# Performance work log

Measured on AMD Instinct MI355X. Metric: run time of the kernel, lower is better.

Reference implementation:

```python
import jax, jax.numpy as jnp
import numpy as np

EMBED_DIM = 768
FFN_DIM = 3072
N_WIRES = 10


def setup_inputs() -> dict:
    key = jax.random.key(0)
    ks = jax.random.split(key, 7)
    x = jax.random.normal(ks[0], (8, 2048, EMBED_DIM), dtype=jnp.float32)
    # map_to_wires: nn.Linear(embed_dim, n_wires, bias=False) -> weight [n_wires, embed_dim]
    W_map = jax.random.normal(ks[1], (N_WIRES, EMBED_DIM), dtype=jnp.float32) / np.sqrt(EMBED_DIM)
    # trainable RY rotation angles, one per wire
    theta = jax.random.uniform(ks[2], (N_WIRES,), dtype=jnp.float32, minval=-np.pi, maxval=np.pi)
    W1 = jax.random.normal(ks[3], (FFN_DIM, N_WIRES), dtype=jnp.float32) / np.sqrt(N_WIRES)
    b1 = jnp.zeros((FFN_DIM,), dtype=jnp.float32)
    W2 = jax.random.normal(ks[4], (EMBED_DIM, FFN_DIM), dtype=jnp.float32) / np.sqrt(FFN_DIM)
    b2 = jnp.zeros((EMBED_DIM,), dtype=jnp.float32)
    return {"x": x, "W_map": W_map, "theta": theta, "W1": W1, "b1": b1, "W2": W2, "b2": b2}


def reference(x, W_map, theta, W1, b1, W2, b2):
    batch, seq_len, embed_dim = x.shape
    x_flat = x.reshape(batch * seq_len, embed_dim)            # [F, E]
    x_wires = x_flat @ W_map.T                                 # [F, W]
    # Quantum circuit: per wire i, state RY(theta_i) RX(x_i) |0>.
    # All gates are single-qubit on the |0...0> product state, so the
    # register stays a product state and <Z_i> reduces exactly to
    # cos(theta_i) * cos(x_i) (same math as the full 2^n statevector sim).
    q_out = jnp.cos(theta)[None, :] * jnp.cos(x_wires)         # [F, W]
    h = jax.nn.relu(q_out @ W1.T + b1)                         # [F, FFN]
    out = h @ W2.T + b2                                        # [F, E]
    return out.reshape(batch, seq_len, embed_dim)
```

## Files before the change

### kernel.cpp

```cpp
#include <hip/hip_runtime.h>
#include <hip/hip_bf16.h>


typedef __attribute__((ext_vector_type(4))) float f32x4;
typedef __attribute__((ext_vector_type(8))) short bf16x8;

#define F_TOTAL 16384
#define E_DIM   768
#define FFN     3072

static __device__ __forceinline__ unsigned short f2bf(float f) {
    union { float f; unsigned int i; } v; v.f = f;
    unsigned int r = v.i + 0x7FFFu + ((v.i >> 16) & 1u);
    return (unsigned short)(r >> 16);
}
static __device__ __forceinline__ unsigned int pkbf(float a, float b) {
    __hip_bfloat162 h2 = __float22bfloat162_rn(float2{a, b});
    union { __hip_bfloat162 h; unsigned int u; } v; v.h = h2; return v.u;
}
static __device__ __forceinline__ void gload16(const void* g, void* l) {
    __builtin_amdgcn_global_load_lds((const __attribute__((address_space(1))) unsigned int*)g,
                                     (__attribute__((address_space(3))) unsigned int*)l,
                                     16, 0, 0);
}

__global__ __launch_bounds__(256) void kPre(const float* __restrict__ x,
                                            const float* __restrict__ wm,
                                            const float* __restrict__ th,
                                            const float* __restrict__ w1,
                                            const float* __restrict__ b1,
                                            const float* __restrict__ w2,
                                            unsigned short* __restrict__ w2b,
                                            unsigned short* __restrict__ w1p,
                                            unsigned short* __restrict__ qp) {
    __shared__ float wms[10 * 768];
    const int bid = (int)blockIdx.x;
    const int tid = (int)threadIdx.x;

    if (bid < 768) {
        const int n = bid;
#pragma unroll
        for (int c0 = 0; c0 < 2; ++c0) {
            int c = tid + c0 * 256;
            if (c < 384) {
                const float4* src = (const float4*)(w2 + (size_t)n * FFN + c * 8);
                float4 a = src[0], b = src[1];
                bf16x8 v;
                v[0] = (short)f2bf(a.x); v[1] = (short)f2bf(a.y);
                v[2] = (short)f2bf(a.z); v[3] = (short)f2bf(a.w);
                v[4] = (short)f2bf(b.x); v[5] = (short)f2bf(b.y);
                v[6] = (short)f2bf(b.z); v[7] = (short)f2bf(b.w);
                *(bf16x8*)(w2b + (size_t)n * FFN + (size_t)(c ^ (n & 7)) * 8) = v;
            }
        }
        return;
    }
    if (bid < 780) {
        int k = (bid - 768) * 256 + tid;
        if (k < FFN) {
            float r[32];
#pragma unroll
            for (int w = 0; w < 10; ++w) r[w] = w1[k * 10 + w];
            r[10] = b1[k];
#pragma unroll
            for (int w = 11; w < 32; ++w) r[w] = 0.f;
#pragma unroll
            for (int c = 0; c < 4; ++c) {
                bf16x8 v;
#pragma unroll
                for (int e = 0; e < 8; ++e) v[e] = (short)f2bf(r[c * 8 + e]);
                *(bf16x8*)(w1p + (size_t)k * 32 + (size_t)((c ^ (k & 3)) * 8)) = v;
            }
        }
        return;
    }

    for (int i = tid; i < 10 * 768; i += 256) wms[i] = wm[i];
    __syncthreads();

    const int wv = tid >> 6, l = tid & 63;
    const int mbase = (bid - 780) * 16 + wv * 4;
    const float thv = (l < 10) ? th[l] : 0.f;
    const float cth = __cosf(thv);

#pragma unroll
    for (int r = 0; r < 4; ++r) {
        const int m = mbase + r;
        const float4* xp = (const float4*)(x + (size_t)m * E_DIM);
        const float4 xa = xp[l], xb = xp[64 + l], xc = xp[128 + l];
        float s[10];
#pragma unroll
        for (int w = 0; w < 10; ++w) {
            const float4* wp = (const float4*)(wms + w * E_DIM);
            const float4 wa = wp[l], wb = wp[64 + l], wc = wp[128 + l];
            float t0 = xa.x * wa.x;
            float t1 = xa.y * wa.y;
            t0 = fmaf(xa.z, wa.z, t0); t1 = fmaf(xa.w, wa.w, t1);
            t0 = fmaf(xb.x, wb.x, t0); t1 = fmaf(xb.y, wb.y, t1);
            t0 = fmaf(xb.z, wb.z, t0); t1 = fmaf(xb.w, wb.w, t1);
            t0 = fmaf(xc.x, wc.x, t0); t1 = fmaf(xc.y, wc.y, t1);
            t0 = fmaf(xc.z, wc.z, t0); t1 = fmaf(xc.w, wc.w, t1);
            s[w] = t0 + t1;
        }
#pragma unroll
        for (int w = 0; w < 10; ++w) {
            float v = s[w];
            v += __shfl_xor(v, 1);  v += __shfl_xor(v, 2);  v += __shfl_xor(v, 4);
            v += __shfl_xor(v, 8);  v += __shfl_xor(v, 16); v += __shfl_xor(v, 32);
            s[w] = v;
        }
        if (l < 32) {
            float sv = 0.f;
#pragma unroll
            for (int w = 0; w < 10; ++w) sv = (l == w) ? s[w] : sv;
            float val = (l < 10) ? (cth * __cosf(sv)) : ((l == 10) ? 1.0f : 0.f);
            qp[(size_t)m * 32 + (size_t)((((l >> 3) ^ (m & 3)) * 8) + (l & 7))] = f2bf(val);
        }
    }
}

__global__ __launch_bounds__(512, 4) void kG(const unsigned short* __restrict__ w2b,
                                             const float* __restrict__ b2,
                                             const unsigned short* __restrict__ qp,
                                             const unsigned short* __restrict__ w1p,
                                             float* __restrict__ outp) {
    __shared__ __align__(16) unsigned short w2s[2][192 * 64];
    __shared__ __align__(16) unsigned short hs[128 * 64];

    const int tid = (int)threadIdx.x;
    const int wv = tid >> 6, l = tid & 63;
    const int bid = (int)blockIdx.x;
    const int x8 = bid & 7, yb = bid >> 3;
    const int m0 = ((x8 & 1) * 64 + yb) * 128;
    const int n0 = (x8 >> 1) * 192;

    const int rw = tid >> 3, cw = tid & 7;
    const int wr = wv >> 2, wc = wv & 3;
    const int par = wv & 1;

    int hwo[4];
    {
        const int hm = wv * 16 + (l & 15);
        const int kb = (l >> 4) * 4;
#pragma unroll
        for (int ki = 0; ki < 4; ++ki) {
            int k = ki * 16 + kb;
            int c = k >> 3;
            hwo[ki] = hm * 64 + ((c ^ (hm & 7)) * 8) + (k & 7);
        }
    }

#define STAGE(BUF, KT) do { int k0_ = (KT) * 64;                                   \
    _Pragma("unroll") for (int i_ = 0; i_ < 3; ++i_) {                             \
        int r_ = i_ * 64 + rw;                                                     \
        gload16(w2b + (size_t)(n0 + r_) * FFN + k0_ + (size_t)cw * 8,              \
                (unsigned short*)w2s[BUF] + i_ * 4096 + wv * 512); } } while (0)

#define LOADW1(D, KT, KI) do {                                                     \
    const unsigned short* a_ = w1p + (size_t)((KT) * 64 + (KI) * 16 + (l & 15)) * 32 \
                                   + (size_t)(((l >> 4) ^ (l & 3)) * 8);           \
    asm volatile("global_load_dwordx4 %0, %1, off" : "=v"(D) : "v"(a_)); } while (0)

    bf16x8 aq;
    {
        const unsigned short* qa = qp + (size_t)(m0 + wv * 16 + (l & 15)) * 32
                                      + (size_t)(((l >> 4) ^ (l & 3)) * 8);
        asm volatile("global_load_dwordx4 %0, %1, off" : "=v"(aq) : "v"(qa));
    }
    bf16x8 f0, f1, f2, f3, g0, g1, g2, g3;
    STAGE(0, 0);
    LOADW1(f0, 0, 0); LOADW1(f1, 0, 1); LOADW1(f2, 0, 2); LOADW1(f3, 0, 3);

    const f32x4 z4 = {0.f, 0.f, 0.f, 0.f};
    f32x4 acc[4][3];
#pragma unroll
    for (int a = 0; a < 4; ++a)
#pragma unroll
        for (int b = 0; b < 3; ++b) acc[a][b] = z4;

    int cur = 0;
    for (int t = 0; t < 48; ++t) {
        asm volatile("s_waitcnt vmcnt(0)" ::: "memory");
        __builtin_amdgcn_sched_barrier(0);
        __builtin_amdgcn_s_barrier();
        __builtin_amdgcn_sched_barrier(0);

        if (t < 47) {
            STAGE(cur ^ 1, t + 1);
            LOADW1(g0, t + 1, 0); LOADW1(g1, t + 1, 1);
            LOADW1(g2, t + 1, 2); LOADW1(g3, t + 1, 3);
        }

        {
            f32x4 hv0 = __builtin_amdgcn_mfma_f32_16x16x32_bf16(f0, aq, z4, 0, 0, 0);
            f32x4 hv1 = __builtin_amdgcn_mfma_f32_16x16x32_bf16(f1, aq, z4, 0, 0, 0);
            f32x4 hv2 = __builtin_amdgcn_mfma_f32_16x16x32_bf16(f2, aq, z4, 0, 0, 0);
            f32x4 hv3 = __builtin_amdgcn_mfma_f32_16x16x32_bf16(f3, aq, z4, 0, 0, 0);
            uint2 pw;
            pw.x = pkbf(fmaxf(hv0[0], 0.f), fmaxf(hv0[1], 0.f));
            pw.y = pkbf(fmaxf(hv0[2], 0.f), fmaxf(hv0[3], 0.f));
            *(uint2*)(hs + hwo[0]) = pw;
            pw.x = pkbf(fmaxf(hv1[0], 0.f), fmaxf(hv1[1], 0.f));
            pw.y = pkbf(fmaxf(hv1[2], 0.f), fmaxf(hv1[3], 0.f));
            *(uint2*)(hs + hwo[1]) = pw;
            pw.x = pkbf(fmaxf(hv2[0], 0.f), fmaxf(hv2[1], 0.f));
            pw.y = pkbf(fmaxf(hv2[2], 0.f), fmaxf(hv2[3], 0.f));
            *(uint2*)(hs + hwo[2]) = pw;
            pw.x = pkbf(fmaxf(hv3[0], 0.f), fmaxf(hv3[1], 0.f));
            pw.y = pkbf(fmaxf(hv3[2], 0.f), fmaxf(hv3[3], 0.f));
            *(uint2*)(hs + hwo[3]) = pw;
        }

        asm volatile("s_waitcnt lgkmcnt(0)" ::: "memory");
        __builtin_amdgcn_sched_barrier(0);
        __builtin_amdgcn_s_barrier();
        __builtin_amdgcn_sched_barrier(0);

        {
            const unsigned short* w2c = (const unsigned short*)w2s[cur];
#pragma unroll
            for (int kx = 0; kx < 2; ++kx) {
                const int win = kx ^ par;
                const int kc = win * 4 + (l >> 4);
                bf16x8 af[4], bfr[3];
#pragma unroll
                for (int mi = 0; mi < 4; ++mi) {
                    int m_ = wr * 64 + mi * 16 + (l & 15);
                    af[mi] = *(const bf16x8*)(hs + m_ * 64 + ((kc ^ (m_ & 7)) * 8));
                }
#pragma unroll
                for (int ni = 0; ni < 3; ++ni) {
                    int n_ = wc * 48 + ni * 16 + (l & 15);
                    bfr[ni] = *(const bf16x8*)(w2c + n_ * 64 + ((kc ^ (n_ & 7)) * 8));
                }
                __builtin_amdgcn_s_setprio(1);
#pragma unroll
                for (int ni = 0; ni < 3; ++ni)
#pragma unroll
                    for (int mi = 0; mi < 4; ++mi)
                        acc[mi][ni] = __builtin_amdgcn_mfma_f32_16x16x32_bf16(af[mi], bfr[ni], acc[mi][ni], 0, 0, 0);
                __builtin_amdgcn_s_setprio(0);
            }
        }

        f0 = g0; f1 = g1; f2 = g2; f3 = g3;
        cur ^= 1;
    }
#undef STAGE
#undef LOADW1

#pragma unroll
    for (int ni = 0; ni < 3; ++ni) {
        int n = n0 + wc * 48 + ni * 16 + (l & 15);
        float b2v = b2[n];
#pragma unroll
        for (int mi = 0; mi < 4; ++mi) {
            int mb = m0 + wr * 64 + mi * 16 + (l >> 4) * 4;
#pragma unroll
            for (int jj = 0; jj < 4; ++jj)
                outp[(size_t)(mb + jj) * E_DIM + n] = acc[mi][ni][jj] + b2v;
        }
    }
}

extern "C" void kernel_launch(void* const* d_in, const int* in_sizes, int n_in,
                              void* d_out, int out_size, void* d_ws, size_t ws_size,
                              hipStream_t stream) {
    const float* x    = (const float*)d_in[0];
    const float* wmap = (const float*)d_in[1];
    const float* th   = (const float*)d_in[2];
    const float* w1   = (const float*)d_in[3];
    const float* b1   = (const float*)d_in[4];
    const float* w2   = (const float*)d_in[5];
    const float* b2   = (const float*)d_in[6];
    float* out = (float*)d_out;

    unsigned short* qp  = (unsigned short*)d_ws;
    unsigned short* w1p = qp + (size_t)F_TOTAL * 32;
    unsigned short* w2b = w1p + (size_t)FFN * 32;

    kPre<<<1804, 256, 0, stream>>>(x, wmap, th, w1, b1, w2, w2b, w1p, qp);
    kG<<<512, 512, 0, stream>>>(w2b, b2, qp, w1p, out);
}
```

Baseline: 120.2 us.

## Software-pipeline first-GEMM h computation one step ahead with 2x unrolled loop

Restructures the fused FFN k-loop so the small first GEMM (W1 x q, ReLU, bf16 pack) for step t+1 runs after the main W2 MFMA phase of step t. Its packed results are held in registers and written to LDS at the start of the next step, and W1 fragments are prefetched two steps ahead. The loop is unrolled by two with fixed buffer indices, which removes the register copies and the cur toggle. W1 and q loads now use plain C++ loads instead of inline asm, so the compiler can schedule them. The goal is to take the h-tile MFMA latency off the critical path between barriers, at the cost of more live registers.

```diff
diff --git a/kernel.cpp b/kernel.cpp
--- a/kernel.cpp
+++ b/kernel.cpp
@@ -150,104 +150,112 @@
         }
     }
 
+    const unsigned short* p1 = w1p + (l & 15) * 32 + ((l >> 4) ^ (l & 3)) * 8;
+
 #define STAGE(BUF, KT) do { int k0_ = (KT) * 64;                                   \
     _Pragma("unroll") for (int i_ = 0; i_ < 3; ++i_) {                             \
         int r_ = i_ * 64 + rw;                                                     \
         gload16(w2b + (size_t)(n0 + r_) * FFN + k0_ + (size_t)cw * 8,              \
                 (unsigned short*)w2s[BUF] + i_ * 4096 + wv * 512); } } while (0)
 
-#define LOADW1(D, KT, KI) do {                                                     \
-    const unsigned short* a_ = w1p + (size_t)((KT) * 64 + (KI) * 16 + (l & 15)) * 32 \
-                                   + (size_t)(((l >> 4) ^ (l & 3)) * 8);           \
-    asm volatile("global_load_dwordx4 %0, %1, off" : "=v"(D) : "v"(a_)); } while (0)
-
-    bf16x8 aq;
-    {
-        const unsigned short* qa = qp + (size_t)(m0 + wv * 16 + (l & 15)) * 32
-                                      + (size_t)(((l >> 4) ^ (l & 3)) * 8);
-        asm volatile("global_load_dwordx4 %0, %1, off" : "=v"(aq) : "v"(qa));
-    }
+#define LOADW1C(D0, D1, D2, D3, KT) do {                                           \
+    const unsigned short* pn_ = p1 + (size_t)(KT) * 2048;                          \
+    D0 = *(const bf16x8*)(pn_);                                                    \
+    D1 = *(const bf16x8*)(pn_ + 512);                                              \
+    D2 = *(const bf16x8*)(pn_ + 1024);                                             \
+    D3 = *(const bf16x8*)(pn_ + 1536);                                             \
+} while (0)
+
+#define HCOMP(W0, W1_, W2_, W3_) do {                                              \
+    f32x4 hv_;                                                                     \
+    hv_ = __builtin_amdgcn_mfma_f32_16x16x32_bf16(W0, aq, z4, 0, 0, 0);            \
+    hp0.x = pkbf(fmaxf(hv_[0],0.f), fmaxf(hv_[1],0.f));                            \
+    hp0.y = pkbf(fmaxf(hv_[2],0.f), fmaxf(hv_[3],0.f));                            \
+    hv_ = __builtin_amdgcn_mfma_f32_16x16x32_bf16(W1_, aq, z4, 0, 0, 0);           \
+    hp1.x = pkbf(fmaxf(hv_[0],0.f), fmaxf(hv_[1],0.f));                            \
+    hp1.y = pkbf(fmaxf(hv_[2],0.f), fmaxf(hv_[3],0.f));                            \
+    hv_ = __builtin_amdgcn_mfma_f32_16x16x32_bf16(W2_, aq, z4, 0, 0, 0);           \
+    hp2.x = pkbf(fmaxf(hv_[0],0.f), fmaxf(hv_[1],0.f));                            \
+    hp2.y = pkbf(fmaxf(hv_[2],0.f), fmaxf(hv_[3],0.f));                            \
+    hv_ = __builtin_amdgcn_mfma_f32_16x16x32_bf16(W3_, aq, z4, 0, 0, 0);           \
+    hp3.x = pkbf(fmaxf(hv_[0],0.f), fmaxf(hv_[1],0.f));                            \
+    hp3.y = pkbf(fmaxf(hv_[2],0.f), fmaxf(hv_[3],0.f));                            \
+} while (0)
+
+#define MAINPH(BUF) do {                                                           \
+    const unsigned short* w2c = (const unsigned short*)w2s[BUF];                   \
+    _Pragma("unroll")                                                              \
+    for (int kx = 0; kx < 2; ++kx) {                                               \
+        const int win = kx ^ par;                                                  \
+        const int kc = win * 4 + (l >> 4);                                         \
+        bf16x8 af[4], bfr[3];                                                      \
+        _Pragma("unroll")                                                          \
+        for (int mi = 0; mi < 4; ++mi) {                                           \
+            int m_ = wr * 64 + mi * 16 + (l & 15);                                 \
+            af[mi] = *(const bf16x8*)(hs + m_ * 64 + ((kc ^ (m_ & 7)) * 8));       \
+        }                                                                          \
+        _Pragma("unroll")                                                          \
+        for (int ni = 0; ni < 3; ++ni) {                                           \
+            int n_ = wc * 48 + ni * 16 + (l & 15);                                 \
+            bfr[ni] = *(const bf16x8*)(w2c + n_ * 64 + ((kc ^ (n_ & 7)) * 8));     \
+        }                                                                          \
+        __builtin_amdgcn_s_setprio(1);                                             \
+        _Pragma("unroll")                                                          \
+        for (int ni = 0; ni < 3; ++ni)                                             \
+            _Pragma("unroll")                                                      \
+            for (int mi = 0; mi < 4; ++mi)                                         \
+                acc[mi][ni] = __builtin_amdgcn_mfma_f32_16x16x32_bf16(             \
+                    af[mi], bfr[ni], acc[mi][ni], 0, 0, 0);                        \
+        __builtin_amdgcn_s_setprio(0);                                             \
+    }                                                                              \
+} while (0)
+
+#define KSTEP(T, BUF, C0, C1, C2, C3, N0, N1, N2, N3) do {                         \
+    asm volatile("s_waitcnt vmcnt(0)" ::: "memory");                               \
+    __builtin_amdgcn_sched_barrier(0);                                             \
+    __builtin_amdgcn_s_barrier();                                                  \
+    __builtin_amdgcn_sched_barrier(0);                                             \
+    if ((T) < 47) STAGE((BUF) ^ 1, (T) + 1);                                       \
+    *(uint2*)(hs + hwo[0]) = hp0;                                                  \
+    *(uint2*)(hs + hwo[1]) = hp1;                                                  \
+    *(uint2*)(hs + hwo[2]) = hp2;                                                  \
+    *(uint2*)(hs + hwo[3]) = hp3;                                                  \
+    if ((T) < 46) LOADW1C(N0, N1, N2, N3, (T) + 2);                                \
+    asm volatile("s_waitcnt lgkmcnt(0)" ::: "memory");                             \
+    __builtin_amdgcn_sched_barrier(0);                                             \
+    __builtin_amdgcn_s_barrier();                                                  \
+    __builtin_amdgcn_sched_barrier(0);                                             \
+    if ((T) < 47) HCOMP(C0, C1, C2, C3);                                           \
+    MAINPH(BUF);                                                                   \
+} while (0)
+
+    bf16x8 aq = *(const bf16x8*)(qp + (size_t)(m0 + wv * 16 + (l & 15)) * 32
+                                    + (size_t)(((l >> 4) ^ (l & 3)) * 8));
     bf16x8 f0, f1, f2, f3, g0, g1, g2, g3;
+    const f32x4 z4 = {0.f, 0.f, 0.f, 0.f};
+    uint2 hp0, hp1, hp2, hp3;
+
     STAGE(0, 0);
-    LOADW1(f0, 0, 0); LOADW1(f1, 0, 1); LOADW1(f2, 0, 2); LOADW1(f3, 0, 3);
-
-    const f32x4 z4 = {0.f, 0.f, 0.f, 0.f};
+    LOADW1C(f0, f1, f2, f3, 0);
+    HCOMP(f0, f1, f2, f3);
+    LOADW1C(g0, g1, g2, g3, 1);
+
     f32x4 acc[4][3];
 #pragma unroll
     for (int a = 0; a < 4; ++a)
 #pragma unroll
         for (int b = 0; b < 3; ++b) acc[a][b] = z4;
 
-    int cur = 0;
-    for (int t = 0; t < 48; ++t) {
-        asm volatile("s_waitcnt vmcnt(0)" ::: "memory");
-        __builtin_amdgcn_sched_barrier(0);
-        __builtin_amdgcn_s_barrier();
-        __builtin_amdgcn_sched_barrier(0);
-
-        if (t < 47) {
-            STAGE(cur ^ 1, t + 1);
-            LOADW1(g0, t + 1, 0); LOADW1(g1, t + 1, 1);
-            LOADW1(g2, t + 1, 2); LOADW1(g3, t + 1, 3);
-        }
-
-        {
-            f32x4 hv0 = __builtin_amdgcn_mfma_f32_16x16x32_bf16(f0, aq, z4, 0, 0, 0);
-            f32x4 hv1 = __builtin_amdgcn_mfma_f32_16x16x32_bf16(f1, aq, z4, 0, 0, 0);
-            f32x4 hv2 = __builtin_amdgcn_mfma_f32_16x16x32_bf16(f2, aq, z4, 0, 0, 0);
-            f32x4 hv3 = __builtin_amdgcn_mfma_f32_16x16x32_bf16(f3, aq, z4, 0, 0, 0);
-            uint2 pw;
-            pw.x = pkbf(fmaxf(hv0[0], 0.f), fmaxf(hv0[1], 0.f));
-            pw.y = pkbf(fmaxf(hv0[2], 0.f), fmaxf(hv0[3], 0.f));
-            *(uint2*)(hs + hwo[0]) = pw;
-            pw.x = pkbf(fmaxf(hv1[0], 0.f), fmaxf(hv1[1], 0.f));
-            pw.y = pkbf(fmaxf(hv1[2], 0.f), fmaxf(hv1[3], 0.f));
-            *(uint2*)(hs + hwo[1]) = pw;
-            pw.x = pkbf(fmaxf(hv2[0], 0.f), fmaxf(hv2[1], 0.f));
-            pw.y = pkbf(fmaxf(hv2[2], 0.f), fmaxf(hv2[3], 0.f));
-            *(uint2*)(hs + hwo[2]) = pw;
-            pw.x = pkbf(fmaxf(hv3[0], 0.f), fmaxf(hv3[1], 0.f));
-            pw.y = pkbf(fmaxf(hv3[2], 0.f), fmaxf(hv3[3], 0.f));
-            *(uint2*)(hs + hwo[3]) = pw;
-        }
-
-        asm volatile("s_waitcnt lgkmcnt(0)" ::: "memory");
-        __builtin_amdgcn_sched_barrier(0);
-        __builtin_amdgcn_s_barrier();
-        __builtin_amdgcn_sched_barrier(0);
-
-        {
-            const unsigned short* w2c = (const unsigned short*)w2s[cur];
-#pragma unroll
-            for (int kx = 0; kx < 2; ++kx) {
-                const int win = kx ^ par;
-                const int kc = win * 4 + (l >> 4);
-                bf16x8 af[4], bfr[3];
-#pragma unroll
-                for (int mi = 0; mi < 4; ++mi) {
-                    int m_ = wr * 64 + mi * 16 + (l & 15);
-                    af[mi] = *(const bf16x8*)(hs + m_ * 64 + ((kc ^ (m_ & 7)) * 8));
-                }
-#pragma unroll
-                for (int ni = 0; ni < 3; ++ni) {
-                    int n_ = wc * 48 + ni * 16 + (l & 15);
-                    bfr[ni] = *(const bf16x8*)(w2c + n_ * 64 + ((kc ^ (n_ & 7)) * 8));
-                }
-                __builtin_amdgcn_s_setprio(1);
-#pragma unroll
-                for (int ni = 0; ni < 3; ++ni)
-#pragma unroll
-                    for (int mi = 0; mi < 4; ++mi)
-                        acc[mi][ni] = __builtin_amdgcn_mfma_f32_16x16x32_bf16(af[mi], bfr[ni], acc[mi][ni], 0, 0, 0);
-                __builtin_amdgcn_s_setprio(0);
-            }
-        }
-
-        f0 = g0; f1 = g1; f2 = g2; f3 = g3;
-        cur ^= 1;
-    }
+#pragma unroll 1
+    for (int tt = 0; tt < 24; ++tt) {
+        KSTEP(2 * tt,     0, g0, g1, g2, g3, f0, f1, f2, f3);
+        KSTEP(2 * tt + 1, 1, f0, f1, f2, f3, g0, g1, g2, g3);
+    }
+#undef KSTEP
+#undef MAINPH
+#undef HCOMP
+#undef LOADW1C
 #undef STAGE
-#undef LOADW1
 
 #pragma unroll
     for (int ni = 0; ni < 3; ++ni) {
```

Result: slower. 304.6 us (+153.3%).
